# Optimization experiments

Measured on AMD Instinct MI355X. Metric: run time of the kernel, lower is better.

The kernel has to match this reference:

```python
import jax, jax.numpy as jnp
import numpy as np

N, H, W, C = 4, 128, 128, 128
G = 8
GC = C // G
K = 9  # 3x3 deformable kernel
PAD = 1
HIN, WIN = H + 2 * PAD, W + 2 * PAD
EPS = 1e-5
OFFSET_SCALE = 1.0


def ln(x, g, b):
    m = jnp.mean(x, -1, keepdims=True)
    v = jnp.mean((x - m) ** 2, -1, keepdims=True)
    return (x - m) * jax.lax.rsqrt(v + EPS) * g + b


def gelu(x):
    return jax.nn.gelu(x, approximate=False)


def dcn_core(xp, offset, mask):
    # xp: (N,H,W,C) value features; offset: (N,H,W,G*K*2); mask: (N,H,W,G,K)
    xpad = jnp.pad(xp, ((0, 0), (PAD, PAD), (PAD, PAD), (0, 0)))
    img = xpad.reshape(N, HIN * WIN, G, GC)
    # reference points normalized by padded size (matches dcnv3_core_pytorch)
    ref_x = (jnp.arange(W, dtype=jnp.float32) + 1.5) / WIN  # (dil*(k-1))//2 + 0.5
    ref_y = (jnp.arange(H, dtype=jnp.float32) + 1.5) / HIN
    RX, RY = jnp.meshgrid(ref_x, ref_y)  # (H,W), xy indexing
    ref = jnp.stack([RX, RY], -1)  # (H,W,2) as (x,y)
    gx, gy = jnp.meshgrid(jnp.linspace(-1.0, 1.0, 3), jnp.linspace(-1.0, 1.0, 3), indexing='ij')
    grid = jnp.stack([gx / WIN, gy / HIN], -1).reshape(K, 2)  # dilation grid, x-major
    off = offset.reshape(N, H, W, G, K, 2)
    loc = (ref[None, :, :, None, None, :] + grid * OFFSET_SCALE
           + off * OFFSET_SCALE / jnp.array([WIN, HIN], jnp.float32))  # (N,H,W,G,K,2)
    # grid_sample align_corners=False pixel coords
    px = loc[..., 0] * WIN - 0.5
    py = loc[..., 1] * HIN - 0.5
    x0 = jnp.floor(px); y0 = jnp.floor(py)
    tx = px - x0; ty = py - y0
    x0i = x0.astype(jnp.int32); y0i = y0.astype(jnp.int32)
    x1i = x0i + 1; y1i = y0i + 1

    def gather(iy, ix):
        valid = ((iy >= 0) & (iy < HIN) & (ix >= 0) & (ix < WIN)).astype(xp.dtype)
        idx = jnp.clip(iy, 0, HIN - 1) * WIN + jnp.clip(ix, 0, WIN - 1)  # (N,H,W,G,K)
        idxf = idx.transpose(0, 1, 2, 4, 3).reshape(N, H * W * K, G, 1)
        v = jnp.take_along_axis(img, idxf, axis=1).reshape(N, H, W, K, G, GC)
        return v * valid.transpose(0, 1, 2, 4, 3)[..., None]

    acc = jnp.zeros((N, H, W, G, GC), xp.dtype)
    for iy, ix, wgt in ((y0i, x0i, (1 - ty) * (1 - tx)),
                        (y0i, x1i, (1 - ty) * tx),
                        (y1i, x0i, ty * (1 - tx)),
                        (y1i, x1i, ty * tx)):
        wm = (wgt * mask).transpose(0, 1, 2, 4, 3)[..., None]  # (N,H,W,K,G,1)
        acc = acc + jnp.sum(gather(iy, ix) * wm, axis=3)  # (N,H,W,G,GC)
    return acc.reshape(N, H, W, C)


def dcn(x, in_w, in_b, dw_k, dw_b, dwln_g, dwln_b, off_w, off_b, mask_w, mask_b, out_w, out_b):
    xp = x @ in_w + in_b  # input_proj
    # offset/mask branch: depthwise 3x3 conv on raw input, LN, GELU
    xc = jax.lax.conv_general_dilated(
        x, dw_k.reshape(3, 3, 1, C), (1, 1), 'SAME',
        dimension_numbers=('NHWC', 'HWIO', 'NHWC'), feature_group_count=C) + dw_b
    x1 = gelu(ln(xc, dwln_g, dwln_b))
    offset = x1 @ off_w + off_b  # (N,H,W,G*K*2)
    mask = jax.nn.softmax((x1 @ mask_w + mask_b).reshape(N, H, W, G, K), axis=-1)
    y = dcn_core(xp, offset, mask)
    return y @ out_w + out_b


def _forward(x, ln1_g, ln1_b, in_w, in_b, dw_k, dw_b, dwln_g, dwln_b, off_w, off_b,
             mask_w, mask_b, out_w, out_b, ln2_g, ln2_b, fc1_w, fc1_b, fc2_w, fc2_b):
    # pre-norm, no layer_scale, no drop_path (rate 0)
    x = x + dcn(ln(x, ln1_g, ln1_b), in_w, in_b, dw_k, dw_b, dwln_g, dwln_b,
                off_w, off_b, mask_w, mask_b, out_w, out_b)
    h = ln(x, ln2_g, ln2_b)
    h = gelu(h @ fc1_w + fc1_b) @ fc2_w + fc2_b
    return x + h


def setup_inputs() -> dict:
    key = jax.random.key(0)
    ks = jax.random.split(key, 10)

    def lin(k, fin, fout, scale=1.0):
        s = scale / np.sqrt(fin)
        return jax.random.uniform(k, (fin, fout), minval=-s, maxval=s, dtype=jnp.float32)

    d = {}
    d['x'] = jax.random.normal(ks[0], (N, H, W, C), dtype=jnp.float32)
    d['ln1_g'] = jnp.ones((C,), jnp.float32); d['ln1_b'] = jnp.zeros((C,), jnp.float32)
    d['in_w'] = lin(ks[1], C, C); d['in_b'] = jnp.zeros((C,), jnp.float32)
    d['dw_k'] = jax.random.normal(ks[2], (3, 3, C), dtype=jnp.float32) * 0.05
    d['dw_b'] = jnp.zeros((C,), jnp.float32)
    d['dwln_g'] = jnp.ones((C,), jnp.float32); d['dwln_b'] = jnp.zeros((C,), jnp.float32)
    d['off_w'] = lin(ks[3], C, G * K * 2, 0.1); d['off_b'] = jnp.zeros((G * K * 2,), jnp.float32)
    d['mask_w'] = lin(ks[4], C, G * K, 0.1); d['mask_b'] = jnp.zeros((G * K,), jnp.float32)
    d['out_w'] = lin(ks[5], C, C); d['out_b'] = jnp.zeros((C,), jnp.float32)
    d['ln2_g'] = jnp.ones((C,), jnp.float32); d['ln2_b'] = jnp.zeros((C,), jnp.float32)
    d['fc1_w'] = lin(ks[6], C, 4 * C); d['fc1_b'] = jnp.zeros((4 * C,), jnp.float32)
    d['fc2_w'] = lin(ks[7], 4 * C, C); d['fc2_b'] = jnp.zeros((C,), jnp.float32)
    return d


def reference(x, ln1_g, ln1_b, in_w, in_b, dw_k, dw_b, dwln_g, dwln_b, off_w, off_b,
              mask_w, mask_b, out_w, out_b, ln2_g, ln2_b, fc1_w, fc1_b, fc2_w, fc2_b):
    return _forward(x, ln1_g, ln1_b, in_w, in_b, dw_k, dw_b, dwln_g, dwln_b, off_w, off_b,
                    mask_w, mask_b, out_w, out_b, ln2_g, ln2_b, fc1_w, fc1_b, fc2_w, fc2_b)
```

## Files before the change

### kernel.cpp

```cpp
#include <hip/hip_runtime.h>
#include <hip/hip_bf16.h>
#include <math.h>

#define NB 4
#define HH 128
#define WW 128
#define CC 128
#define GG 8
#define GCC 16
#define KK 9
#define NHW (NB*HH*WW)

typedef __hip_bfloat16 bf16;
typedef __attribute__((ext_vector_type(8))) short short8;
typedef __attribute__((ext_vector_type(4))) float f32x4;

__device__ __forceinline__ float b2f(bf16 v){ return __bfloat162float(v); }
__device__ __forceinline__ bf16 f2b(float v){ return __float2bfloat16(v); }
__device__ __forceinline__ float gelu_f(float v){
  float x = fabsf(v) * 0.70710678118654752f;
  float t = __builtin_amdgcn_rcpf(fmaf(0.3275911f, x, 1.0f));
  float p = t*fmaf(t, fmaf(t, fmaf(t, fmaf(t, 1.061405429f, -1.453152027f),
                         1.421413741f), -0.284496736f), 0.254829592f);
  float e = __expf(-x*x);
  float er = copysignf(fmaf(-p, e, 1.0f), v);
  return 0.5f*v*(1.0f+er);
}
__device__ __forceinline__ float lo_bf(unsigned u){ union{unsigned i; float f;} c; c.i = u<<16; return c.f; }
__device__ __forceinline__ float hi_bf(unsigned u){ union{unsigned i; float f;} c; c.i = u&0xffff0000u; return c.f; }
__device__ __forceinline__ unsigned pk(float a, float b){
  return ((unsigned)__bfloat16_as_ushort(f2b(b))<<16) | (unsigned)__bfloat16_as_ushort(f2b(a));
}
__device__ __forceinline__ void st_out(bf16* p, float v){ *p = f2b(v); }
__device__ __forceinline__ void st_out(float* p, float v){ *p = v; }
__device__ __forceinline__ void acc8(float* a, uint4 u, float w){
  a[0]+=w*lo_bf(u.x); a[1]+=w*hi_bf(u.x); a[2]+=w*lo_bf(u.y); a[3]+=w*hi_bf(u.y);
  a[4]+=w*lo_bf(u.z); a[5]+=w*hi_bf(u.z); a[6]+=w*lo_bf(u.w); a[7]+=w*hi_bf(u.w);
}

__global__ __launch_bounds__(256) void prep_k(
    const float* __restrict__ inw,  const float* __restrict__ outw,
    const float* __restrict__ fc1w, const float* __restrict__ fc2w,
    const float* __restrict__ offw, const float* __restrict__ offb,
    const float* __restrict__ maskw,const float* __restrict__ maskb,
    bf16* __restrict__ inwt, bf16* __restrict__ outwt,
    bf16* __restrict__ w1t,  bf16* __restrict__ w2t,
    bf16* __restrict__ wsw,  float* __restrict__ cw)
{
  int idx = blockIdx.x*256 + threadIdx.x;
  if (idx < 16384){
    int n = idx>>7, k = idx&127;
    inwt[idx] = f2b(inw[(size_t)k*128 + n]);
  } else if (idx < 32768){
    int i = idx-16384; int n = i>>7, k = i&127;
    outwt[i] = f2b(outw[(size_t)k*128 + n]);
  } else if (idx < 98304){
    int i = idx-32768; int n = i>>7, k = i&127;
    w1t[i] = f2b(fc1w[(size_t)k*512 + n]);
  } else if (idx < 163840){
    int i = idx-98304; int n = i>>9, k = i&511;
    w2t[i] = f2b(fc2w[(size_t)k*128 + n]);
  } else if (idx < 192512){
    int i = idx-163840; int nn = i>>7, k = i&127;
    float v = (nn<144) ? offw[(size_t)k*144+nn] : (nn<216 ? maskw[(size_t)k*72+(nn-144)] : 0.f);
    wsw[i] = f2b(v);
  } else if (idx < 192736){
    int i = idx-192512;
    cw[i] = (i<144) ? offb[i] : (i<216 ? maskb[i-144] : 0.f);
  }
}

__global__ __launch_bounds__(256) void ln_k(const float* __restrict__ X,
    const float* __restrict__ gam, const float* __restrict__ bet, bf16* __restrict__ Y)
{
  int lane = threadIdx.x & 63;
  int wid  = threadIdx.x >> 6;
  size_t pix = (size_t)blockIdx.x*4 + wid;
  const float* xp = X + pix*CC;
  int c0 = lane*2;
  float v0 = xp[c0], v1 = xp[c0+1];
  float s = v0+v1, ss = v0*v0+v1*v1;
  #pragma unroll
  for (int off=32; off>0; off>>=1){ s += __shfl_xor(s,off,64); ss += __shfl_xor(ss,off,64); }
  float mean = s*(1.f/CC);
  float var  = ss*(1.f/CC) - mean*mean;
  float rstd = rsqrtf(var + 1e-5f);
  float y0 = (v0-mean)*rstd*gam[c0]   + bet[c0];
  float y1 = (v1-mean)*rstd*gam[c0+1] + bet[c0+1];
  Y[pix*CC + c0]   = f2b(y0);
  Y[pix*CC + c0+1] = f2b(y1);
}

__global__ __launch_bounds__(256) void convln_k(const bf16* __restrict__ XN,
    const float* __restrict__ dwk, const float* __restrict__ dwb,
    const float* __restrict__ gam, const float* __restrict__ bet, bf16* __restrict__ X1)
{
  int tid = threadIdx.x;
  int px = tid>>4, cg = tid&15;
  int ch0 = cg*8;
  int pix = blockIdx.x*16 + px;
  int w = pix & (WW-1), h = (pix>>7)&(HH-1), n = pix>>14;
  float acc[8];
  {
    float4 b0 = *(const float4*)(dwb + ch0), b1 = *(const float4*)(dwb + ch0 + 4);
    acc[0]=b0.x; acc[1]=b0.y; acc[2]=b0.z; acc[3]=b0.w;
    acc[4]=b1.x; acc[5]=b1.y; acc[6]=b1.z; acc[7]=b1.w;
  }
  #pragma unroll
  for (int ky=0;ky<3;ky++){
    int yy = h+ky-1; if ((unsigned)yy>=(unsigned)HH) continue;
    #pragma unroll
    for (int kx=0;kx<3;kx++){
      int xx = w+kx-1; if ((unsigned)xx>=(unsigned)WW) continue;
      uint4 u = *(const uint4*)(XN + ((size_t)((n*HH+yy)*WW+xx))*CC + ch0);
      const float* wp = dwk + (ky*3+kx)*CC + ch0;
      float4 w0 = *(const float4*)wp; float4 w1 = *(const float4*)(wp+4);
      acc[0] += lo_bf(u.x)*w0.x; acc[1] += hi_bf(u.x)*w0.y;
      acc[2] += lo_bf(u.y)*w0.z; acc[3] += hi_bf(u.y)*w0.w;
      acc[4] += lo_bf(u.z)*w1.x; acc[5] += hi_bf(u.z)*w1.y;
      acc[6] += lo_bf(u.w)*w1.z; acc[7] += hi_bf(u.w)*w1.w;
    }
  }
  float s=0.f, ss=0.f;
  #pragma unroll
  for (int i=0;i<8;i++){ s += acc[i]; ss += acc[i]*acc[i]; }
  #pragma unroll
  for (int off=1; off<16; off<<=1){ s += __shfl_xor(s,off,64); ss += __shfl_xor(ss,off,64); }
  float mean=s*(1.f/CC), var=ss*(1.f/CC)-mean*mean, rstd=rsqrtf(var+1e-5f);
  float4 g0 = *(const float4*)(gam + ch0), g1 = *(const float4*)(gam + ch0 + 4);
  float4 be0 = *(const float4*)(bet + ch0), be1 = *(const float4*)(bet + ch0 + 4);
  float gv[8] = {g0.x,g0.y,g0.z,g0.w,g1.x,g1.y,g1.z,g1.w};
  float bv[8] = {be0.x,be0.y,be0.z,be0.w,be1.x,be1.y,be1.z,be1.w};
  float o[8];
  #pragma unroll
  for (int i=0;i<8;i++) o[i] = gelu_f((acc[i]-mean)*rstd*gv[i] + bv[i]);
  uint4 up; up.x = pk(o[0],o[1]); up.y = pk(o[2],o[3]); up.z = pk(o[4],o[5]); up.w = pk(o[6],o[7]);
  *(uint4*)(X1 + (size_t)pix*CC + ch0) = up;
}

#define OMS 226
__global__ __launch_bounds__(256) void samp_k(const bf16* __restrict__ X1,
    const bf16* __restrict__ XP,
    const bf16* __restrict__ wsw, const float* __restrict__ cw,
    bf16* __restrict__ Y)
{
  __shared__ bf16 oms[32*OMS];
  int tid = threadIdx.x;
  int pix0 = blockIdx.x*32;
  int wave = tid>>6, l = tid&63, lo16 = l&15, quad = l>>4;
  int nt0 = wave*4;
  int ntn = (wave==3) ? 2 : 4;
  short8 af[2][4];
  #pragma unroll
  for (int mt=0;mt<2;mt++)
    #pragma unroll
    for (int ks=0;ks<4;ks++)
      af[mt][ks] = *(const short8*)(X1 + (size_t)(pix0+mt*16+lo16)*128 + ks*32 + quad*8);
  f32x4 z = {0.f,0.f,0.f,0.f};
  f32x4 acc[2][4];
  #pragma unroll
  for (int mt=0;mt<2;mt++)
    #pragma unroll
    for (int t=0;t<4;t++) acc[mt][t]=z;
  for (int t=0;t<ntn;t++){
    int nt = nt0+t;
    #pragma unroll
    for (int ks=0;ks<4;ks++){
      short8 bfr = *(const short8*)(wsw + (size_t)(nt*16+lo16)*128 + ks*32 + quad*8);
      acc[0][t] = __builtin_amdgcn_mfma_f32_16x16x32_bf16(af[0][ks], bfr, acc[0][t], 0,0,0);
      acc[1][t] = __builtin_amdgcn_mfma_f32_16x16x32_bf16(af[1][ks], bfr, acc[1][t], 0,0,0);
    }
  }
  for (int t=0;t<ntn;t++){
    int col = (nt0+t)*16 + lo16;
    float bb = cw[col];
    #pragma unroll
    for (int mt=0;mt<2;mt++)
      #pragma unroll
      for (int r=0;r<4;r++)
        oms[(mt*16 + quad*4 + r)*OMS + col] = f2b(acc[mt][t][r] + bb);
  }
  __syncthreads();
  {
    int m = tid>>3, g = tid&7;
    int base = m*OMS + 144 + g*9;
    float sc[9]; float mx = -1e30f;
    #pragma unroll
    for (int k=0;k<9;k++){ sc[k] = b2f(oms[base+k]); mx = fmaxf(mx, sc[k]); }
    float sum = 0.f;
    #pragma unroll
    for (int k=0;k<9;k++){ sc[k] = expf(sc[k]-mx); sum += sc[k]; }
    float inv = 1.f/sum;
    #pragma unroll
    for (int k=0;k<9;k++) oms[base+k] = f2b(sc[k]*inv);
  }
  __syncthreads();
  int oct = tid&15, sl = tid>>4;
  int g = oct>>1;
  int ch = g*GCC + (oct&1)*8;
  int w0 = pix0 & (WW-1);
  int h  = (pix0>>7) & (HH-1);
  int n  = pix0>>14;
  const bf16* base = XP + (size_t)n*HH*WW*CC + ch;
  for (int it=0; it<2; it++){
    int m = it*16 + sl;
    int wc = w0 + m;
    const bf16* omrow = &oms[m*OMS];
    float a[8] = {0.f,0.f,0.f,0.f,0.f,0.f,0.f,0.f};
    #pragma unroll
    for (int k=0;k<9;k++){
      float offx = b2f(omrow[g*18 + 2*k]);
      float offy = b2f(omrow[g*18 + 2*k + 1]);
      float mk   = b2f(omrow[144 + g*9 + k]);
      float pxf = (float)(wc + (k/3) - 1) + offx;
      float pyf = (float)(h  + (k%3) - 1) + offy;
      float x0f = floorf(pxf), y0f = floorf(pyf);
      float txf = pxf-x0f,     tyf = pyf-y0f;
      int x0 = (int)x0f, y0 = (int)y0f;
      int x1i = x0+1,    y1i = y0+1;
      float vx0 = ((unsigned)x0 <(unsigned)WW)?1.f:0.f;
      float vx1 = ((unsigned)x1i<(unsigned)WW)?1.f:0.f;
      float vy0 = ((unsigned)y0 <(unsigned)HH)?1.f:0.f;
      float vy1 = ((unsigned)y1i<(unsigned)HH)?1.f:0.f;
      int cx0 = min(max(x0,0),WW-1),  cx1 = min(max(x1i,0),WW-1);
      int cy0 = min(max(y0,0),HH-1),  cy1 = min(max(y1i,0),HH-1);
      float w00=(1.f-tyf)*(1.f-txf)*mk*vy0*vx0, w01=(1.f-tyf)*txf*mk*vy0*vx1;
      float w10=tyf*(1.f-txf)*mk*vy1*vx0,       w11=tyf*txf*mk*vy1*vx1;
      uint4 u00 = *(const uint4*)(base + ((size_t)(cy0*WW+cx0))*CC);
      uint4 u01 = *(const uint4*)(base + ((size_t)(cy0*WW+cx1))*CC);
      uint4 u10 = *(const uint4*)(base + ((size_t)(cy1*WW+cx0))*CC);
      uint4 u11 = *(const uint4*)(base + ((size_t)(cy1*WW+cx1))*CC);
      acc8(a,u00,w00); acc8(a,u01,w01); acc8(a,u10,w10); acc8(a,u11,w11);
    }
    uint4 outp;
    outp.x = pk(a[0],a[1]); outp.y = pk(a[2],a[3]);
    outp.z = pk(a[4],a[5]); outp.w = pk(a[6],a[7]);
    *(uint4*)(Y + (size_t)(pix0+m)*CC + ch) = outp;
  }
}

template<typename OutT, bool RES>
__global__ __launch_bounds__(256) void gemm_mfma(const bf16* __restrict__ A,
    const bf16* __restrict__ Bt, const float* __restrict__ bias,
    const float* __restrict__ res, OutT* __restrict__ C)
{
  int tid = threadIdx.x;
  int wave = tid>>6, l = tid&63, lo16 = l&15, quad = l>>4;
  int m0 = blockIdx.y*256 + wave*64;
  int n0 = blockIdx.x*64;
  short8 bfr[4][4];
  #pragma unroll
  for (int ks=0;ks<4;ks++)
    #pragma unroll
    for (int nt=0;nt<4;nt++)
      bfr[ks][nt] = *(const short8*)(Bt + (size_t)(n0+nt*16+lo16)*128 + ks*32 + quad*8);
  f32x4 z = {0.f,0.f,0.f,0.f};
  f32x4 acc[4][4];
  #pragma unroll
  for (int mt=0;mt<4;mt++)
    #pragma unroll
    for (int nt=0;nt<4;nt++) acc[mt][nt]=z;
  #pragma unroll
  for (int ks=0;ks<4;ks++){
    short8 af[4];
    #pragma unroll
    for (int mt=0;mt<4;mt++)
      af[mt] = *(const short8*)(A + (size_t)(m0+mt*16+lo16)*128 + ks*32 + quad*8);
    #pragma unroll
    for (int nt=0;nt<4;nt++)
      #pragma unroll
      for (int mt=0;mt<4;mt++)
        acc[mt][nt] = __builtin_amdgcn_mfma_f32_16x16x32_bf16(af[mt], bfr[ks][nt], acc[mt][nt], 0,0,0);
  }
  #pragma unroll
  for (int mt=0;mt<4;mt++)
    #pragma unroll
    for (int nt=0;nt<4;nt++){
      int col = n0 + nt*16 + lo16;
      float bb = bias[col];
      #pragma unroll
      for (int r=0;r<4;r++){
        int row = m0 + mt*16 + quad*4 + r;
        float v = acc[mt][nt][r] + bb;
        if (RES) v += res[(size_t)row*128 + col];
        st_out(&C[(size_t)row*128 + col], v);
      }
    }
}

__global__ __launch_bounds__(256) void mlp_mfma(const float* __restrict__ X2,
    const float* __restrict__ lng, const float* __restrict__ lnb,
    const bf16* __restrict__ w1t, const float* __restrict__ b1,
    const bf16* __restrict__ w2t, const float* __restrict__ b2,
    float* __restrict__ OUT)
{
  __shared__ __align__(16) char smem[34816 + 18432];
  bf16* h0s = (bf16*)smem;
  bf16* ts  = (bf16*)smem;
  bf16* w1s = (bf16*)(smem + 34816);
  bf16* w2s = (bf16*)(smem + 34816);
  int tid = threadIdx.x;
  int wave = tid>>6, l = tid&63, lo16 = l&15, quad = l>>4;
  int m0 = blockIdx.x*128;
  #pragma unroll
  for (int itn=0; itn<2; itn++){
    int px = (tid>>2) + itn*64;
    int q = tid&3;
    const float* xr = X2 + (size_t)(m0+px)*128 + q*32;
    float v[32];
    #pragma unroll
    for (int i=0;i<8;i++) *(float4*)(v+i*4) = *(const float4*)(xr+i*4);
    float s=0.f, ss=0.f;
    #pragma unroll
    for (int i=0;i<32;i++){ s += v[i]; ss += v[i]*v[i]; }
    s  += __shfl_xor(s,1,64);  ss += __shfl_xor(ss,1,64);
    s  += __shfl_xor(s,2,64);  ss += __shfl_xor(ss,2,64);
    float mean = s*(1.f/CC), var = ss*(1.f/CC)-mean*mean, rstd = rsqrtf(var+1e-5f);
    const float* gp = lng + q*32; const float* bp = lnb + q*32;
    uint4* dst = (uint4*)(&h0s[px*136 + q*32]);
    #pragma unroll
    for (int i=0;i<4;i++){
      float4 g0 = *(const float4*)(gp+i*8),  g1 = *(const float4*)(gp+i*8+4);
      float4 c0v = *(const float4*)(bp+i*8), c1v = *(const float4*)(bp+i*8+4);
      float o0 = (v[i*8+0]-mean)*rstd*g0.x + c0v.x;
      float o1 = (v[i*8+1]-mean)*rstd*g0.y + c0v.y;
      float o2 = (v[i*8+2]-mean)*rstd*g0.z + c0v.z;
      float o3 = (v[i*8+3]-mean)*rstd*g0.w + c0v.w;
      float o4 = (v[i*8+4]-mean)*rstd*g1.x + c1v.x;
      float o5 = (v[i*8+5]-mean)*rstd*g1.y + c1v.y;
      float o6 = (v[i*8+6]-mean)*rstd*g1.z + c1v.z;
      float o7 = (v[i*8+7]-mean)*rstd*g1.w + c1v.w;
      uint4 up; up.x = pk(o0,o1); up.y = pk(o2,o3); up.z = pk(o4,o5); up.w = pk(o6,o7);
      dst[i] = up;
    }
  }
  __syncthreads();
  short8 a1[2][4];
  #pragma unroll
  for (int mt=0;mt<2;mt++)
    #pragma unroll
    for (int ks=0;ks<4;ks++)
      a1[mt][ks] = *(const short8*)(&h0s[(wave*32 + mt*16 + lo16)*136 + ks*32 + quad*8]);
  f32x4 z = {0.f,0.f,0.f,0.f};
  f32x4 acc2[2][8];
  #pragma unroll
  for (int mt=0;mt<2;mt++)
    #pragma unroll
    for (int nt=0;nt<8;nt++) acc2[mt][nt]=z;

  for (int c0=0;c0<512;c0+=64){
    __syncthreads();
    #pragma unroll
    for (int it=0;it<4;it++){
      int e = it*2048 + tid*8;
      int nn = e>>7, kk = e&127;
      *(uint4*)(&w1s[nn*136 + kk]) = *(const uint4*)(w1t + (size_t)(c0+nn)*128 + kk);
    }
    __syncthreads();
    f32x4 acc1[2][4];
    #pragma unroll
    for (int mt=0;mt<2;mt++)
      #pragma unroll
      for (int nt=0;nt<4;nt++) acc1[mt][nt]=z;
    #pragma unroll
    for (int ks=0;ks<4;ks++)
      #pragma unroll
      for (int nt=0;nt<4;nt++){
        short8 bfr = *(const short8*)(&w1s[(nt*16+lo16)*136 + ks*32 + quad*8]);
        acc1[0][nt] = __builtin_amdgcn_mfma_f32_16x16x32_bf16(a1[0][ks], bfr, acc1[0][nt], 0,0,0);
        acc1[1][nt] = __builtin_amdgcn_mfma_f32_16x16x32_bf16(a1[1][ks], bfr, acc1[1][nt], 0,0,0);
      }
    #pragma unroll
    for (int mt=0;mt<2;mt++)
      #pragma unroll
      for (int nt=0;nt<4;nt++){
        float bb = b1[c0 + nt*16 + lo16];
        #pragma unroll
        for (int r=0;r<4;r++)
          ts[(wave*32 + mt*16 + quad*4 + r)*72 + nt*16 + lo16] = f2b(gelu_f(acc1[mt][nt][r] + bb));
      }
    __syncthreads();
    #pragma unroll
    for (int it=0;it<4;it++){
      int e = it*2048 + tid*8;
      int nn = e>>6, kk = e&63;
      *(uint4*)(&w2s[nn*72 + kk]) = *(const uint4*)(w2t + (size_t)nn*512 + c0 + kk);
    }
    __syncthreads();
    #pragma unroll
    for (int ks2=0;ks2<2;ks2++){
      short8 a2[2];
      #pragma unroll
      for (int mt=0;mt<2;mt++)
        a2[mt] = *(const short8*)(&ts[(wave*32 + mt*16 + lo16)*72 + ks2*32 + quad*8]);
      #pragma unroll
      for (int nt2=0;nt2<8;nt2++){
        short8 bfr2 = *(const short8*)(&w2s[(nt2*16+lo16)*72 + ks2*32 + quad*8]);
        acc2[0][nt2] = __builtin_amdgcn_mfma_f32_16x16x32_bf16(a2[0], bfr2, acc2[0][nt2], 0,0,0);
        acc2[1][nt2] = __builtin_amdgcn_mfma_f32_16x16x32_bf16(a2[1], bfr2, acc2[1][nt2], 0,0,0);
      }
    }
  }
  #pragma unroll
  for (int mt=0;mt<2;mt++)
    #pragma unroll
    for (int nt=0;nt<8;nt++){
      int col = nt*16 + lo16;
      float bb = b2[col];
      #pragma unroll
      for (int r=0;r<4;r++){
        int row = m0 + wave*32 + mt*16 + quad*4 + r;
        float v = acc2[mt][nt][r] + bb + X2[(size_t)row*128 + col];
        OUT[(size_t)row*128 + col] = v;
      }
    }
}

extern "C" void kernel_launch(void* const* d_in, const int* in_sizes, int n_in,
                              void* d_out, int out_size, void* d_ws, size_t ws_size,
                              hipStream_t stream)
{
  const float* x    = (const float*)d_in[0];
  const float* ln1g = (const float*)d_in[1];
  const float* ln1b = (const float*)d_in[2];
  const float* inw  = (const float*)d_in[3];
  const float* inb  = (const float*)d_in[4];
  const float* dwk  = (const float*)d_in[5];
  const float* dwb  = (const float*)d_in[6];
  const float* dwlng= (const float*)d_in[7];
  const float* dwlnb= (const float*)d_in[8];
  const float* offw = (const float*)d_in[9];
  const float* offb = (const float*)d_in[10];
  const float* maskw= (const float*)d_in[11];
  const float* maskb= (const float*)d_in[12];
  const float* outw = (const float*)d_in[13];
  const float* outb = (const float*)d_in[14];
  const float* ln2g = (const float*)d_in[15];
  const float* ln2b = (const float*)d_in[16];
  const float* fc1w = (const float*)d_in[17];
  const float* fc1b = (const float*)d_in[18];
  const float* fc2w = (const float*)d_in[19];
  const float* fc2b = (const float*)d_in[20];
  float* out = (float*)d_out;

  bf16* ws = (bf16*)d_ws;
  const size_t S = (size_t)NHW*CC;
  bf16* xn = ws;
  bf16* xp = ws + S;
  bf16* x1 = ws + 2*S;
  bf16* y  = xn;
  float* x2 = out;
  bf16* inwt  = ws + 3*S;
  bf16* outwt = inwt + 128*128;
  bf16* w1t   = outwt + 128*128;
  bf16* w2t   = w1t + 512*128;
  bf16* wsw   = w2t + 128*512;
  float* cw   = (float*)(wsw + 224*128);

  prep_k<<<753, 256, 0, stream>>>(inw, outw, fc1w, fc2w, offw, offb, maskw, maskb,
                                  inwt, outwt, w1t, w2t, wsw, cw);
  ln_k<<<NHW/4, 256, 0, stream>>>(x, ln1g, ln1b, xn);
  gemm_mfma<bf16,false><<<dim3(2,256), 256, 0, stream>>>(xn, inwt, inb, nullptr, xp);
  convln_k<<<NHW/16, 256, 0, stream>>>(xn, dwk, dwb, dwlng, dwlnb, x1);
  samp_k<<<NHW/32, 256, 0, stream>>>(x1, xp, wsw, cw, y);
  gemm_mfma<float,true><<<dim3(2,256), 256, 0, stream>>>(y, outwt, outb, x, x2);
  mlp_mfma<<<NHW/128, 256, 0, stream>>>(x2, ln2g, ln2b, w1t, fc1b, w2t, fc2b, out);
}
```

Baseline: 282.3 us.

## Fuse output projection and residual into the MLP kernel

The separate output-projection GEMM launch is removed. Its work (y @ out_w + bias + residual x) now runs inside the MLP kernel, which keeps x2 in registers, computes LayerNorm2 from the MFMA accumulator layout with cross-lane shuffles, and reuses x2 for the final residual. This drops one kernel launch and the fp32 x2 round trip through global memory. The cost is more register pressure in the MLP kernel (16 extra accumulator vectors) and an extra shared-memory weight load per block.

```diff
diff --git a/kernel.cpp b/kernel.cpp
--- a/kernel.cpp
+++ b/kernel.cpp
@@ -288,13 +288,16 @@
     }
 }
 
-__global__ __launch_bounds__(256) void mlp_mfma(const float* __restrict__ X2,
+__global__ __launch_bounds__(256) void mlp_fused(const bf16* __restrict__ Yb,
+    const float* __restrict__ X, const bf16* __restrict__ owt,
+    const float* __restrict__ ob,
     const float* __restrict__ lng, const float* __restrict__ lnb,
     const bf16* __restrict__ w1t, const float* __restrict__ b1,
     const bf16* __restrict__ w2t, const float* __restrict__ b2,
     float* __restrict__ OUT)
 {
   __shared__ __align__(16) char smem[34816 + 18432];
+  bf16* ows = (bf16*)smem;
   bf16* h0s = (bf16*)smem;
   bf16* ts  = (bf16*)smem;
   bf16* w1s = (bf16*)(smem + 34816);
@@ -302,46 +305,75 @@
   int tid = threadIdx.x;
   int wave = tid>>6, l = tid&63, lo16 = l&15, quad = l>>4;
   int m0 = blockIdx.x*128;
-  #pragma unroll
-  for (int itn=0; itn<2; itn++){
-    int px = (tid>>2) + itn*64;
-    int q = tid&3;
-    const float* xr = X2 + (size_t)(m0+px)*128 + q*32;
-    float v[32];
-    #pragma unroll
-    for (int i=0;i<8;i++) *(float4*)(v+i*4) = *(const float4*)(xr+i*4);
-    float s=0.f, ss=0.f;
-    #pragma unroll
-    for (int i=0;i<32;i++){ s += v[i]; ss += v[i]*v[i]; }
-    s  += __shfl_xor(s,1,64);  ss += __shfl_xor(ss,1,64);
-    s  += __shfl_xor(s,2,64);  ss += __shfl_xor(ss,2,64);
-    float mean = s*(1.f/CC), var = ss*(1.f/CC)-mean*mean, rstd = rsqrtf(var+1e-5f);
-    const float* gp = lng + q*32; const float* bp = lnb + q*32;
-    uint4* dst = (uint4*)(&h0s[px*136 + q*32]);
-    #pragma unroll
-    for (int i=0;i<4;i++){
-      float4 g0 = *(const float4*)(gp+i*8),  g1 = *(const float4*)(gp+i*8+4);
-      float4 c0v = *(const float4*)(bp+i*8), c1v = *(const float4*)(bp+i*8+4);
-      float o0 = (v[i*8+0]-mean)*rstd*g0.x + c0v.x;
-      float o1 = (v[i*8+1]-mean)*rstd*g0.y + c0v.y;
-      float o2 = (v[i*8+2]-mean)*rstd*g0.z + c0v.z;
-      float o3 = (v[i*8+3]-mean)*rstd*g0.w + c0v.w;
-      float o4 = (v[i*8+4]-mean)*rstd*g1.x + c1v.x;
-      float o5 = (v[i*8+5]-mean)*rstd*g1.y + c1v.y;
-      float o6 = (v[i*8+6]-mean)*rstd*g1.z + c1v.z;
-      float o7 = (v[i*8+7]-mean)*rstd*g1.w + c1v.w;
-      uint4 up; up.x = pk(o0,o1); up.y = pk(o2,o3); up.z = pk(o4,o5); up.w = pk(o6,o7);
-      dst[i] = up;
-    }
+  f32x4 z = {0.f,0.f,0.f,0.f};
+
+  #pragma unroll
+  for (int it=0;it<8;it++){
+    int e = it*2048 + tid*8;
+    int nn = e>>7, kk = e&127;
+    *(uint4*)(&ows[nn*136 + kk]) = *(const uint4*)(owt + (size_t)nn*128 + kk);
   }
   __syncthreads();
+  f32x4 x2a[2][8];
+  #pragma unroll
+  for (int mt=0;mt<2;mt++)
+    #pragma unroll
+    for (int nt=0;nt<8;nt++) x2a[mt][nt]=z;
+  #pragma unroll
+  for (int ks=0;ks<4;ks++){
+    short8 ay[2];
+    #pragma unroll
+    for (int mt=0;mt<2;mt++)
+      ay[mt] = *(const short8*)(Yb + (size_t)(m0+wave*32+mt*16+lo16)*128 + ks*32 + quad*8);
+    #pragma unroll
+    for (int nt=0;nt<8;nt++){
+      short8 bfr = *(const short8*)(&ows[(nt*16+lo16)*136 + ks*32 + quad*8]);
+      x2a[0][nt] = __builtin_amdgcn_mfma_f32_16x16x32_bf16(ay[0], bfr, x2a[0][nt], 0,0,0);
+      x2a[1][nt] = __builtin_amdgcn_mfma_f32_16x16x32_bf16(ay[1], bfr, x2a[1][nt], 0,0,0);
+    }
+  }
+  #pragma unroll
+  for (int mt=0;mt<2;mt++)
+    #pragma unroll
+    for (int nt=0;nt<8;nt++){
+      int col = nt*16 + lo16;
+      float bb = ob[col];
+      #pragma unroll
+      for (int r=0;r<4;r++){
+        int row = m0 + wave*32 + mt*16 + quad*4 + r;
+        x2a[mt][nt][r] += bb + X[(size_t)row*128 + col];
+      }
+    }
+  __syncthreads();
+
+  {
+    float gv[8], bvv[8];
+    #pragma unroll
+    for (int nt=0;nt<8;nt++){ gv[nt] = lng[nt*16+lo16]; bvv[nt] = lnb[nt*16+lo16]; }
+    #pragma unroll
+    for (int mt=0;mt<2;mt++)
+      #pragma unroll
+      for (int r=0;r<4;r++){
+        float s=0.f, ss=0.f;
+        #pragma unroll
+        for (int nt=0;nt<8;nt++){ float v = x2a[mt][nt][r]; s += v; ss += v*v; }
+        s += __shfl_xor(s,1,64);  ss += __shfl_xor(ss,1,64);
+        s += __shfl_xor(s,2,64);  ss += __shfl_xor(ss,2,64);
+        s += __shfl_xor(s,4,64);  ss += __shfl_xor(ss,4,64);
+        s += __shfl_xor(s,8,64);  ss += __shfl_xor(ss,8,64);
+        float mean = s*(1.f/CC), var = ss*(1.f/CC)-mean*mean, rstd = rsqrtf(var+1e-5f);
+        int rowl = wave*32 + mt*16 + quad*4 + r;
+        #pragma unroll
+        for (int nt=0;nt<8;nt++)
+          h0s[rowl*136 + nt*16 + lo16] = f2b((x2a[mt][nt][r]-mean)*rstd*gv[nt] + bvv[nt]);
+      }
+  }
   short8 a1[2][4];
   #pragma unroll
   for (int mt=0;mt<2;mt++)
     #pragma unroll
     for (int ks=0;ks<4;ks++)
       a1[mt][ks] = *(const short8*)(&h0s[(wave*32 + mt*16 + lo16)*136 + ks*32 + quad*8]);
-  f32x4 z = {0.f,0.f,0.f,0.f};
   f32x4 acc2[2][8];
   #pragma unroll
   for (int mt=0;mt<2;mt++)
@@ -410,8 +442,7 @@
       #pragma unroll
       for (int r=0;r<4;r++){
         int row = m0 + wave*32 + mt*16 + quad*4 + r;
-        float v = acc2[mt][nt][r] + bb + X2[(size_t)row*128 + col];
-        OUT[(size_t)row*128 + col] = v;
+        OUT[(size_t)row*128 + col] = acc2[mt][nt][r] + bb + x2a[mt][nt][r];
       }
     }
 }
@@ -449,7 +480,6 @@
   bf16* xp = ws + S;
   bf16* x1 = ws + 2*S;
   bf16* y  = xn;
-  float* x2 = out;
   bf16* inwt  = ws + 3*S;
   bf16* outwt = inwt + 128*128;
   bf16* w1t   = outwt + 128*128;
@@ -463,6 +493,6 @@
   gemm_mfma<bf16,false><<<dim3(2,256), 256, 0, stream>>>(xn, inwt, inb, nullptr, xp);
   convln_k<<<NHW/16, 256, 0, stream>>>(xn, dwk, dwb, dwlng, dwlnb, x1);
   samp_k<<<NHW/32, 256, 0, stream>>>(x1, xp, wsw, cw, y);
-  gemm_mfma<float,true><<<dim3(2,256), 256, 0, stream>>>(y, outwt, outb, x, x2);
-  mlp_mfma<<<NHW/128, 256, 0, stream>>>(x2, ln2g, ln2b, w1t, fc1b, w2t, fc2b, out);
-}
+  mlp_fused<<<NHW/128, 256, 0, stream>>>(y, x, outwt, outb, ln2g, ln2b,
+                                         w1t, fc1b, w2t, fc2b, out);
+}
```

Measured after the change: 312.8 us. 10.8% more time.
